# Performance work log

Hardware: AMD Instinct MI355X
Metric: run time of the kernel (lower is better)

## Reference

```python
import jax, jax.numpy as jnp
import numpy as np

B, N, DIM = 2, 2048, 2048
HEADS, DIM_HEAD = 16, 64
INNER = HEADS * DIM_HEAD  # 1024, != DIM -> to_out projection active
SCALE = DIM_HEAD ** -0.5


def setup_inputs() -> dict:
    key = jax.random.key(0)
    ks = jax.random.split(key, 10)
    s_in = 1.0 / np.sqrt(DIM)
    s_out = 1.0 / np.sqrt(INNER)
    return {
        "h_t": jax.random.normal(ks[0], (B, N, DIM), jnp.float32),
        "h_a": jax.random.normal(ks[1], (B, N, DIM), jnp.float32),
        "h_v": jax.random.normal(ks[2], (B, N, DIM), jnp.float32),
        "W_q": jax.random.normal(ks[3], (DIM, INNER), jnp.float32) * s_in,
        "W_k_ta": jax.random.normal(ks[4], (DIM, INNER), jnp.float32) * s_in,
        "W_k_tv": jax.random.normal(ks[5], (DIM, INNER), jnp.float32) * s_in,
        "W_v_ta": jax.random.normal(ks[6], (DIM, INNER), jnp.float32) * s_in,
        "W_v_tv": jax.random.normal(ks[7], (DIM, INNER), jnp.float32) * s_in,
        "W_out": jax.random.normal(ks[8], (INNER, DIM), jnp.float32) * s_out,
        "b_out": jnp.zeros((DIM,), jnp.float32),
    }


def _split_heads(x):
    # [b, n, h*d] -> [b, h, n, d]
    b, n, _ = x.shape
    return x.reshape(b, n, HEADS, DIM_HEAD).transpose(0, 2, 1, 3)


def _cross_attn(q, k, v):
    # q,k,v: [b, h, n, d]
    dots = jnp.einsum('bhid,bhjd->bhij', q, k) * SCALE
    attn = jax.nn.softmax(dots, axis=-1)
    out = jnp.einsum('bhij,bhjd->bhid', attn, v)
    b, h, n, d = out.shape
    return out.transpose(0, 2, 1, 3).reshape(b, n, h * d)  # [b, n, h*d]


def reference(h_t, h_a, h_v, W_q, W_k_ta, W_k_tv, W_v_ta, W_v_tv, W_out, b_out):
    q = _split_heads(h_t @ W_q)
    k_ta = _split_heads(h_a @ W_k_ta)
    v_ta = _split_heads(h_a @ W_v_ta)
    k_tv = _split_heads(h_v @ W_k_tv)
    v_tv = _split_heads(h_v @ W_v_tv)
    out_ta = _cross_attn(q, k_ta, v_ta)
    out_tv = _cross_attn(q, k_tv, v_tv)
    # project_out=True since inner_dim != dim; dropout=0 (eval)
    return h_t + (out_ta + out_tv) @ W_out + b_out
```

## Files before the change

kernel.cpp:

```cpp
#include <hip/hip_runtime.h>
#include <hip/hip_bf16.h>

typedef __attribute__((ext_vector_type(8))) short s16x8;
typedef __attribute__((ext_vector_type(4))) float f32x4;
typedef unsigned short u16;
typedef unsigned int u32;
typedef unsigned long long u64;

__device__ __forceinline__ u16 f2bf(float x) {
  __hip_bfloat16 h = __float2bfloat16(x);
  return *reinterpret_cast<u16*>(&h);
}
__device__ __forceinline__ float bf2f(u16 x) {
  union { u32 u; float f; } c; c.u = ((u32)x) << 16; return c.f;
}
__device__ __forceinline__ u32 pk2(float lo, float hi) {
  return ((u32)f2bf(hi) << 16) | (u32)f2bf(lo);
}

__device__ __forceinline__ void glds16(const void* g, void* lds) {
  __builtin_amdgcn_global_load_lds(
      (const __attribute__((address_space(1))) u32*)(u64)g,
      (__attribute__((address_space(3))) u32*)(u32)(u64)lds, 16, 0, 0);
}

__device__ __forceinline__ void tcast_tile(const float* __restrict__ in,
                                           u16* __restrict__ out,
                                           int R, int C, int ldo,
                                           int bx, int by, int tid,
                                           u16 (*t)[72]) {
  const int c0 = bx * 64, r0 = by * 64;
#pragma unroll
  for (int it = 0; it < 4; ++it) {
    int c = it * 256 + tid;
    int row = c >> 4, sub = c & 15;
    float4 v = *(const float4*)(in + (u64)(r0 + row) * C + c0 + sub * 4);
    t[sub * 4 + 0][row] = f2bf(v.x);
    t[sub * 4 + 1][row] = f2bf(v.y);
    t[sub * 4 + 2][row] = f2bf(v.z);
    t[sub * 4 + 3][row] = f2bf(v.w);
  }
  __syncthreads();
#pragma unroll
  for (int it = 0; it < 2; ++it) {
    int c = it * 256 + tid;
    int orow = c >> 3, osub = c & 7;
    *(s16x8*)(out + (u64)(c0 + orow) * ldo + r0 + osub * 8) =
        *(const s16x8*)&t[orow][osub * 8];
  }
}

__global__ __launch_bounds__(256) void k_prep(
    const float* __restrict__ h_t, const float* __restrict__ h_a,
    const float* __restrict__ h_v, const float* __restrict__ W_q,
    const float* __restrict__ W_k_ta, const float* __restrict__ W_v_ta,
    const float* __restrict__ W_k_tv, const float* __restrict__ W_v_tv,
    const float* __restrict__ W_out, u16* __restrict__ hT,
    u16* __restrict__ hA, u16* __restrict__ hV, u16* __restrict__ WqT,
    u16* __restrict__ WkvTa, u16* __restrict__ WkvTv, u16* __restrict__ WoT) {
  __shared__ u16 t[64][72];
  const int bid = blockIdx.x, tid = threadIdx.x;
  if (bid < 12288) {
    const float* in = bid < 4096 ? h_t : bid < 8192 ? h_a : h_v;
    u16* out = bid < 4096 ? hT : bid < 8192 ? hA : hV;
    const int i = (bid & 4095) * 2048 + tid * 8;
    float4 a = *(const float4*)(in + i);
    float4 b = *(const float4*)(in + i + 4);
    union { s16x8 v; u16 e[8]; } r;
    r.e[0] = f2bf(a.x); r.e[1] = f2bf(a.y); r.e[2] = f2bf(a.z); r.e[3] = f2bf(a.w);
    r.e[4] = f2bf(b.x); r.e[5] = f2bf(b.y); r.e[6] = f2bf(b.z); r.e[7] = f2bf(b.w);
    *(s16x8*)(out + i) = r.v;
  } else if (bid < 14848) {
    const int tt = bid - 12288;
    const int wi = tt / 512, t2 = tt % 512;
    const float* in;
    u16* out;
    switch (wi) {
      case 0: in = W_q;    out = WqT; break;
      case 1: in = W_k_ta; out = WkvTa; break;
      case 2: in = W_v_ta; out = WkvTa + 1024 * 2048; break;
      case 3: in = W_k_tv; out = WkvTv; break;
      default: in = W_v_tv; out = WkvTv + 1024 * 2048; break;
    }
    tcast_tile(in, out, 2048, 1024, 2048, t2 % 16, t2 / 16, tid, t);
  } else {
    const int t2 = bid - 14848;
    tcast_tile(W_out, WoT, 1024, 2048, 1024, t2 % 32, t2 / 32, tid, t);
  }
}

__global__ __launch_bounds__(256) void k_vtrans2(const u16* __restrict__ kva,
                                                 const u16* __restrict__ kvv,
                                                 u16* __restrict__ vta,
                                                 u16* __restrict__ vtv) {
  __shared__ u16 t[64][72];
  const int bx = blockIdx.x, tb = blockIdx.y;
  const int bh = bx & 31;
  const u16* kv = (bx < 32) ? kva : kvv;
  u16* vt = (bx < 32) ? vta : vtv;
  const int b = bh >> 4, h = bh & 15;
  const int tid = threadIdx.x;
  const u16* src = kv + (u64)(b * 2048 + tb * 64) * 2048 + 1024 + h * 64;
#pragma unroll
  for (int it = 0; it < 2; ++it) {
    int c = it * 256 + tid;
    int trow = c >> 3, dsub = c & 7;
    union { s16x8 v; u16 e[8]; } u;
    u.v = *(const s16x8*)(src + (u64)trow * 2048 + dsub * 8);
#pragma unroll
    for (int j = 0; j < 8; ++j) t[dsub * 8 + j][trow] = u.e[j];
  }
  __syncthreads();
  u16* dst = vt + (u64)bh * 64 * 2048 + tb * 64;
#pragma unroll
  for (int it = 0; it < 2; ++it) {
    int c = it * 256 + tid;
    int drow = c >> 3, tsub = c & 7;
    *(s16x8*)(dst + (u64)drow * 2048 + tsub * 8) = *(const s16x8*)&t[drow][tsub * 8];
  }
}

__global__ __launch_bounds__(256) void k_add(const u16* __restrict__ ao,
                                             u16* __restrict__ aoc) {
  const int i = blockIdx.x * 2048 + threadIdx.x * 8;
  const int row = i >> 10, col = i & 1023;
  union { s16x8 v; u16 e[8]; } A, B, O;
  A.v = *(const s16x8*)(ao + (u64)row * 2048 + col);
  B.v = *(const s16x8*)(ao + (u64)row * 2048 + 1024 + col);
#pragma unroll
  for (int j = 0; j < 8; ++j) O.e[j] = f2bf(bf2f(A.e[j]) + bf2f(B.e[j]));
  *(s16x8*)(aoc + (u64)row * 1024 + col) = O.v;
}

template <int TM, int TN, int MODE>
__global__ __launch_bounds__(256) void k_gemm(const u16* __restrict__ A,
                                              const u16* __restrict__ Bt,
                                              void* __restrict__ Cout,
                                              const float* __restrict__ resid,
                                              const float* __restrict__ bias,
                                              int M, int N, int K, float scale) {
  constexpr int MR = TM / 32, NR = TN / 32;
  __shared__ u16 smem[(TM + TN) * 64];
  const int tid = threadIdx.x;
  const int lane = tid & 63, w = tid >> 6;
  const int g = lane >> 4, lr = lane & 15;
  const int wm = (w >> 1) * (TM / 2), wn = (w & 1) * (TN / 2);
  const int m0 = blockIdx.y * TM, n0 = blockIdx.x * TN;

  f32x4 acc[MR][NR] = {};
  int roff[2];
  roff[0] = (g * 16) ^ ((lr & 7) << 4);
  roff[1] = (64 + g * 16) ^ ((lr & 7) << 4);

  const int nkt = K >> 6;
  for (int kt = 0; kt < nkt; ++kt) {
    const int k0 = kt << 6;
#pragma unroll
    for (int it = 0; it < (TM + TN) / 32; ++it) {
      int c = it * 256 + tid;
      int p = c * 16;
      const u16* gsrc;
      if (c < TM * 8) {
        int lby = p ^ (((p >> 7) & 7) << 4);
        gsrc = A + (u64)(m0 + (lby >> 7)) * K + k0 + ((lby >> 4) & 7) * 8;
      } else {
        int pb = p - TM * 128;
        int lby = pb ^ (((pb >> 7) & 7) << 4);
        gsrc = Bt + (u64)(n0 + (lby >> 7)) * K + k0 + ((lby >> 4) & 7) * 8;
      }
      glds16(gsrc, (char*)smem + p);
    }
    __syncthreads();
#pragma unroll
    for (int ks = 0; ks < 2; ++ks) {
      s16x8 a[MR], b[NR];
#pragma unroll
      for (int m = 0; m < MR; ++m)
        a[m] = *(const s16x8*)((const char*)smem + (wm + m * 16 + lr) * 128 + roff[ks]);
#pragma unroll
      for (int n = 0; n < NR; ++n)
        b[n] = *(const s16x8*)((const char*)smem + TM * 128 + (wn + n * 16 + lr) * 128 + roff[ks]);
#pragma unroll
      for (int m = 0; m < MR; ++m)
#pragma unroll
        for (int n = 0; n < NR; ++n)
          acc[m][n] = __builtin_amdgcn_mfma_f32_16x16x32_bf16(a[m], b[n], acc[m][n], 0, 0, 0);
    }
    __syncthreads();
  }

#pragma unroll
  for (int m = 0; m < MR; ++m)
#pragma unroll
    for (int n = 0; n < NR; ++n) {
      const int col = n0 + wn + n * 16 + lr;
#pragma unroll
      for (int r = 0; r < 4; ++r) {
        const int row = m0 + wm + m * 16 + g * 4 + r;
        if constexpr (MODE == 0) {
          ((u16*)Cout)[(u64)row * N + col] = f2bf(acc[m][n][r]);
        } else if constexpr (MODE == 2) {
          ((u16*)Cout)[(u64)row * N + col] = f2bf(acc[m][n][r] * scale);
        } else {
          ((float*)Cout)[(u64)row * N + col] =
              acc[m][n][r] + resid[(u64)row * N + col] + bias[col];
        }
      }
    }
}

__global__ __launch_bounds__(512, 6) void k_attn(const u16* __restrict__ Q,
                                                 const u16* __restrict__ Kta,
                                                 const u16* __restrict__ Ktv,
                                                 const u16* __restrict__ VTta,
                                                 const u16* __restrict__ VTtv,
                                                 u16* __restrict__ AO) {
  const int bx = blockIdx.x;
  const int br = bx & 1, bh = bx >> 1;
  const int b = bh >> 4, h = bh & 15;
  const int qb = blockIdx.y;
  const int tid = threadIdx.x, lane = tid & 63, w = tid >> 6;
  const int g = lane >> 4, q = lane & 15;
  const int qrow = b * 2048 + qb * 128 + w * 16;
  const int bh64 = bh * 64;
  const u16* Kp  = br ? Ktv  : Kta;
  const u16* VTp = br ? VTtv : VTta;

  __shared__ __align__(16) char sbuf[2][16384];
  __shared__ u32 pbuf[8][16][32];

  s16x8 qf[2];
#pragma unroll
  for (int ks = 0; ks < 2; ++ks)
    qf[ks] = *(const s16x8*)(Q + (u64)(qrow + q) * 1024 + h * 64 + ks * 32 + g * 8);

  const int sp = tid * 16;
  const int slby = sp ^ (((sp >> 7) & 7) << 4);
  const int srow = slby >> 7, scol = (slby & 127) >> 1;

  {
    glds16(Kp + (u64)(b * 2048 + 0 + srow) * 2048 + h * 64 + scol, sbuf[0] + sp);
    glds16(VTp + (u64)(bh64 + srow) * 2048 + 0 + scol, sbuf[0] + 8192 + sp);
  }
  __syncthreads();

  float lsum = 0.f;
  f32x4 acco[4] = {};
  const int xsw = (q & 7) << 4;
  const int psw = (q & 7) << 2;

  for (int t = 0; t < 32; ++t) {
    const int cur = t & 1;
    if (t + 1 < 32) {
      const int kv1 = (t + 1) * 64;
      glds16(Kp + (u64)(b * 2048 + kv1 + srow) * 2048 + h * 64 + scol,
             sbuf[cur ^ 1] + sp);
      glds16(VTp + (u64)(bh64 + srow) * 2048 + kv1 + scol,
             sbuf[cur ^ 1] + 8192 + sp);
    }

    f32x4 s[4];
    __builtin_amdgcn_s_setprio(1);
#pragma unroll
    for (int n = 0; n < 4; ++n) {
      const char* base = sbuf[cur] + (16 * n + q) * 128;
      s16x8 kf0 = *(const s16x8*)(base + ((16 * g) ^ xsw));
      s16x8 kf1 = *(const s16x8*)(base + ((64 + 16 * g) ^ xsw));
      f32x4 z = {};
      z = __builtin_amdgcn_mfma_f32_16x16x32_bf16(kf0, qf[0], z, 0, 0, 0);
      s[n] = __builtin_amdgcn_mfma_f32_16x16x32_bf16(kf1, qf[1], z, 0, 0, 0);
    }
    __builtin_amdgcn_s_setprio(0);

#pragma unroll
    for (int n = 0; n < 4; ++n) {
#pragma unroll
      for (int r = 0; r < 4; ++r) s[n][r] = __builtin_amdgcn_exp2f(s[n][r]);
      lsum += (s[n][0] + s[n][1]) + (s[n][2] + s[n][3]);
      pbuf[w][q][(8 * n + 2 * g) ^ psw]     = pk2(s[n][0], s[n][1]);
      pbuf[w][q][(8 * n + 2 * g + 1) ^ psw] = pk2(s[n][2], s[n][3]);
    }
    s16x8 pb[2];
#pragma unroll
    for (int ks = 0; ks < 2; ++ks)
      pb[ks] = *(const s16x8*)&pbuf[w][q][(16 * ks + 4 * g) ^ psw];

    __builtin_amdgcn_s_setprio(1);
#pragma unroll
    for (int n = 0; n < 4; ++n) {
      const char* base = sbuf[cur] + 8192 + (16 * n + q) * 128;
      s16x8 v0 = *(const s16x8*)(base + ((16 * g) ^ xsw));
      s16x8 v1 = *(const s16x8*)(base + ((64 + 16 * g) ^ xsw));
      acco[n] = __builtin_amdgcn_mfma_f32_16x16x32_bf16(v0, pb[0], acco[n], 0, 0, 0);
      acco[n] = __builtin_amdgcn_mfma_f32_16x16x32_bf16(v1, pb[1], acco[n], 0, 0, 0);
    }
    __builtin_amdgcn_s_setprio(0);
    __syncthreads();
  }

  lsum += __shfl_xor(lsum, 16);
  lsum += __shfl_xor(lsum, 32);
  const float inv = 1.0f / lsum;

#pragma unroll
  for (int n = 0; n < 4; ++n) {
    pbuf[w][q][(8 * n + 2 * g) ^ psw]     = pk2(acco[n][0] * inv, acco[n][1] * inv);
    pbuf[w][q][(8 * n + 2 * g + 1) ^ psw] = pk2(acco[n][2] * inv, acco[n][3] * inv);
  }
#pragma unroll
  for (int c = 0; c < 2; ++c) {
    const int row = (lane >> 3) + 8 * c;
    const int wc = (lane & 7) * 4;
    s16x8 vv = *(const s16x8*)&pbuf[w][row][wc ^ ((row & 7) << 2)];
    *(s16x8*)(AO + (u64)(b * 2048 + qb * 128 + w * 16 + row) * 2048 +
              br * 1024 + h * 64 + (lane & 7) * 8) = vv;
  }
}

extern "C" void kernel_launch(void* const* d_in, const int* in_sizes, int n_in,
                              void* d_out, int out_size, void* d_ws, size_t ws_size,
                              hipStream_t stream) {
  (void)in_sizes; (void)n_in; (void)out_size; (void)ws_size;
  const float* h_t    = (const float*)d_in[0];
  const float* h_a    = (const float*)d_in[1];
  const float* h_v    = (const float*)d_in[2];
  const float* W_q    = (const float*)d_in[3];
  const float* W_k_ta = (const float*)d_in[4];
  const float* W_k_tv = (const float*)d_in[5];
  const float* W_v_ta = (const float*)d_in[6];
  const float* W_v_tv = (const float*)d_in[7];
  const float* W_out  = (const float*)d_in[8];
  const float* b_out  = (const float*)d_in[9];
  float* out = (float*)d_out;

  const float CEXP = 0.125f * 1.44269504088896f;

  u16* ws    = (u16*)d_ws;
  u16* hT    = ws;
  u16* hA    = hT + 8388608;
  u16* hV    = hA + 8388608;
  u16* WqT   = hV + 8388608;
  u16* WkvTa = WqT + 2097152;
  u16* WkvTv = WkvTa + 4194304;
  u16* WoT   = WkvTv + 4194304;
  u16* Qb    = WoT + 2097152;
  u16* KVta  = Qb + 4194304;
  u16* KVtv  = KVta + 8388608;
  u16* VTta  = KVtv + 8388608;
  u16* VTtv  = VTta + 4194304;
  u16* AO    = hT;
  u16* AOc   = hA;

  k_prep<<<15360, 256, 0, stream>>>(h_t, h_a, h_v, W_q, W_k_ta, W_v_ta,
                                    W_k_tv, W_v_tv, W_out,
                                    hT, hA, hV, WqT, WkvTa, WkvTv, WoT);

  k_gemm<64, 128, 2><<<dim3(8, 64), 256, 0, stream>>>(hT, WqT, Qb, nullptr, nullptr, 4096, 1024, 2048, CEXP);
  k_gemm<128, 128, 0><<<dim3(16, 32), 256, 0, stream>>>(hA, WkvTa, KVta, nullptr, nullptr, 4096, 2048, 2048, 1.0f);
  k_gemm<128, 128, 0><<<dim3(16, 32), 256, 0, stream>>>(hV, WkvTv, KVtv, nullptr, nullptr, 4096, 2048, 2048, 1.0f);

  k_vtrans2<<<dim3(64, 32), 256, 0, stream>>>(KVta, KVtv, VTta, VTtv);

  k_attn<<<dim3(64, 16), 512, 0, stream>>>(Qb, KVta, KVtv, VTta, VTtv, AO);

  k_add<<<2048, 256, 0, stream>>>(AO, AOc);

  k_gemm<128, 128, 1><<<dim3(16, 32), 256, 0, stream>>>(AOc, WoT, out, h_t, b_out, 4096, 2048, 1024, 1.0f);
}
```

Measured before the change: 302.5 us.

## Single-buffer attention K/V tiles, compute softmax sums via MFMA, raise occupancy

```diff
diff --git a/kernel.cpp b/kernel.cpp
--- a/kernel.cpp
+++ b/kernel.cpp
@@ -209,7 +209,7 @@
     }
 }
 
-__global__ __launch_bounds__(512, 6) void k_attn(const u16* __restrict__ Q,
+__global__ __launch_bounds__(512, 8) void k_attn(const u16* __restrict__ Q,
                                                  const u16* __restrict__ Kta,
                                                  const u16* __restrict__ Ktv,
                                                  const u16* __restrict__ VTta,
@@ -226,44 +226,39 @@
   const u16* Kp  = br ? Ktv  : Kta;
   const u16* VTp = br ? VTtv : VTta;
 
-  __shared__ __align__(16) char sbuf[2][16384];
+  __shared__ __align__(16) char sbuf[16384];
   __shared__ u32 pbuf[8][16][32];
 
   s16x8 qf[2];
 #pragma unroll
   for (int ks = 0; ks < 2; ++ks)
     qf[ks] = *(const s16x8*)(Q + (u64)(qrow + q) * 1024 + h * 64 + ks * 32 + g * 8);
+
+  union { s16x8 v; u16 e[8]; } ones;
+#pragma unroll
+  for (int j = 0; j < 8; ++j) ones.e[j] = 0x3F80;
 
   const int sp = tid * 16;
   const int slby = sp ^ (((sp >> 7) & 7) << 4);
   const int srow = slby >> 7, scol = (slby & 127) >> 1;
 
   {
-    glds16(Kp + (u64)(b * 2048 + 0 + srow) * 2048 + h * 64 + scol, sbuf[0] + sp);
-    glds16(VTp + (u64)(bh64 + srow) * 2048 + 0 + scol, sbuf[0] + 8192 + sp);
+    glds16(Kp + (u64)(b * 2048 + srow) * 2048 + h * 64 + scol, sbuf + sp);
+    glds16(VTp + (u64)(bh64 + srow) * 2048 + scol, sbuf + 8192 + sp);
   }
   __syncthreads();
 
-  float lsum = 0.f;
+  f32x4 lacc = {};
   f32x4 acco[4] = {};
   const int xsw = (q & 7) << 4;
   const int psw = (q & 7) << 2;
 
   for (int t = 0; t < 32; ++t) {
-    const int cur = t & 1;
-    if (t + 1 < 32) {
-      const int kv1 = (t + 1) * 64;
-      glds16(Kp + (u64)(b * 2048 + kv1 + srow) * 2048 + h * 64 + scol,
-             sbuf[cur ^ 1] + sp);
-      glds16(VTp + (u64)(bh64 + srow) * 2048 + kv1 + scol,
-             sbuf[cur ^ 1] + 8192 + sp);
-    }
-
     f32x4 s[4];
     __builtin_amdgcn_s_setprio(1);
 #pragma unroll
     for (int n = 0; n < 4; ++n) {
-      const char* base = sbuf[cur] + (16 * n + q) * 128;
+      const char* base = sbuf + (16 * n + q) * 128;
       s16x8 kf0 = *(const s16x8*)(base + ((16 * g) ^ xsw));
       s16x8 kf1 = *(const s16x8*)(base + ((64 + 16 * g) ^ xsw));
       f32x4 z = {};
@@ -276,7 +271,6 @@
     for (int n = 0; n < 4; ++n) {
 #pragma unroll
       for (int r = 0; r < 4; ++r) s[n][r] = __builtin_amdgcn_exp2f(s[n][r]);
-      lsum += (s[n][0] + s[n][1]) + (s[n][2] + s[n][3]);
       pbuf[w][q][(8 * n + 2 * g) ^ psw]     = pk2(s[n][0], s[n][1]);
       pbuf[w][q][(8 * n + 2 * g + 1) ^ psw] = pk2(s[n][2], s[n][3]);
     }
@@ -286,21 +280,28 @@
       pb[ks] = *(const s16x8*)&pbuf[w][q][(16 * ks + 4 * g) ^ psw];
 
     __builtin_amdgcn_s_setprio(1);
+    lacc = __builtin_amdgcn_mfma_f32_16x16x32_bf16(ones.v, pb[0], lacc, 0, 0, 0);
+    lacc = __builtin_amdgcn_mfma_f32_16x16x32_bf16(ones.v, pb[1], lacc, 0, 0, 0);
 #pragma unroll
     for (int n = 0; n < 4; ++n) {
-      const char* base = sbuf[cur] + 8192 + (16 * n + q) * 128;
+      const char* base = sbuf + 8192 + (16 * n + q) * 128;
       s16x8 v0 = *(const s16x8*)(base + ((16 * g) ^ xsw));
       s16x8 v1 = *(const s16x8*)(base + ((64 + 16 * g) ^ xsw));
       acco[n] = __builtin_amdgcn_mfma_f32_16x16x32_bf16(v0, pb[0], acco[n], 0, 0, 0);
       acco[n] = __builtin_amdgcn_mfma_f32_16x16x32_bf16(v1, pb[1], acco[n], 0, 0, 0);
     }
     __builtin_amdgcn_s_setprio(0);
+
     __syncthreads();
-  }
-
-  lsum += __shfl_xor(lsum, 16);
-  lsum += __shfl_xor(lsum, 32);
-  const float inv = 1.0f / lsum;
+    if (t + 1 < 32) {
+      const int kv1 = (t + 1) * 64;
+      glds16(Kp + (u64)(b * 2048 + kv1 + srow) * 2048 + h * 64 + scol, sbuf + sp);
+      glds16(VTp + (u64)(bh64 + srow) * 2048 + kv1 + scol, sbuf + 8192 + sp);
+    }
+    __syncthreads();
+  }
+
+  const float inv = 1.0f / lacc[0];
 
 #pragma unroll
   for (int n = 0; n < 4; ++n) {
```

Result: slower. 322.6 us (+6.7%).
